# Performance work log

Hardware: AMD Instinct MI355X
Metric: run time of the kernel (lower is better)

## Reference

```python
import jax, jax.numpy as jnp
import numpy as np

N, D, H, DK, DEG = 8192, 512, 8, 64, 16
E = N * DEG
M = N


def setup_inputs() -> dict:
    key = jax.random.key(0)
    ks = jax.random.split(key, 12)
    x = jax.random.normal(ks[0], (N, D), dtype=jnp.float32)
    # every node has DEG neighbors -> sorted row index, random cols
    row_index = jnp.repeat(jnp.arange(N, dtype=jnp.int64), DEG)
    col_index = jax.random.randint(ks[1], (E,), 0, M, dtype=jnp.int64)
    to_col_index = jax.random.randint(ks[2], (M,), 0, N, dtype=jnp.int64)
    att_bias = 0.1 * jax.random.normal(ks[3], (H, E), dtype=jnp.float32)
    pos = 10.0 * jax.random.uniform(ks[4], (N, 3), dtype=jnp.float32)
    col_pos = 10.0 * jax.random.uniform(ks[5], (M, 3), dtype=jnp.float32)
    dist = jnp.linalg.norm(col_pos[col_index] - pos[row_index], axis=-1)
    s = 1.0 / np.sqrt(D)
    Wq = s * jax.random.normal(ks[6], (H, DK, D), dtype=jnp.float32)
    Wqv = s * jax.random.normal(ks[7], (H, 3, D), dtype=jnp.float32)
    Wk = s * jax.random.normal(ks[8], (H, DK, D), dtype=jnp.float32)
    Wv = s * jax.random.normal(ks[9], (H, DK, D), dtype=jnp.float32)
    Wout = s * jax.random.normal(ks[10], (D, D + 4 * H), dtype=jnp.float32)
    bout = jnp.zeros((D,), dtype=jnp.float32)
    return {"x": x, "row_index": row_index, "col_index": col_index,
            "to_col_index": to_col_index, "att_bias": att_bias, "dist": dist,
            "pos": pos, "col_pos": col_pos, "Wq": Wq, "Wqv": Wqv, "Wk": Wk,
            "Wv": Wv, "Wout": Wout, "bout": bout}


def reference(x, row_index, col_index, to_col_index, att_bias, dist, pos,
              col_pos, Wq, Wqv, Wk, Wv, Wout, bout):
    n = x.shape[0]
    dk = Wq.shape[1]
    scale = 1.0 / jnp.sqrt(jnp.asarray(dk, x.dtype))
    # per-head projections: [H, N, dk]
    q = jnp.einsum('nd,hkd->hnk', x, Wq) * scale
    qv = jnp.einsum('nd,hkd->hnk', x, Wqv)              # [H, N, 3]
    kx = jnp.einsum('nd,hkd->hnk', x, Wk)[:, to_col_index]  # [H, M, dk]
    vx = jnp.einsum('nd,hkd->hnk', x, Wv)[:, to_col_index]
    # gather per edge -> [E, H, *]
    qe = q[:, row_index].transpose(1, 0, 2)
    ke = kx[:, col_index].transpose(1, 0, 2)
    qve = qv[:, row_index].transpose(1, 0, 2)           # [E, H, 3]
    rel = col_pos[col_index] - pos[row_index]           # [E, 3]
    dist_e = jnp.where(dist == 0, jnp.inf, dist)        # masked_fill(dist==0, inf)
    # angular = qv_row . col_pos_col - qv_row . pos_row = qv_row . rel
    angular = jnp.einsum('ehc,ec->eh', qve, rel)
    logit = jnp.einsum('ehk,ehk->eh', qe, ke) + att_bias.T + angular / dist_e[:, None]
    # sparse (per-row segment) softmax
    m = jax.ops.segment_max(logit, row_index, num_segments=n)
    p = jnp.exp(logit - m[row_index])
    s = jax.ops.segment_sum(p, row_index, num_segments=n)
    att = p / s[row_index]                              # [E, H]
    natt = att / dist_e[:, None]
    dst_vec = jax.ops.segment_sum(natt[:, :, None] * col_pos[col_index][:, None, :],
                                  row_index, num_segments=n)   # [N, H, 3]
    avg_inv_dist = jax.ops.segment_sum(natt, row_index, num_segments=n)  # [N, H]
    src_vec = avg_inv_dist[:, :, None] * pos[:, None, :]
    diff = dst_vec - src_vec
    feat3 = diff / jnp.maximum(jnp.linalg.norm(diff, axis=-1, keepdims=True), 1e-12)
    ve = vx[:, col_index].transpose(1, 0, 2)            # [E, H, dk]
    y = jax.ops.segment_sum(att[:, :, None] * ve, row_index, num_segments=n)  # [N, H, dk]
    feat = jnp.concatenate([y, feat3, avg_inv_dist[:, :, None]], axis=-1)
    feat = feat.reshape(n, -1)                          # [N, H*(dk+4)]
    return feat @ Wout.T + bout
```

## Files before the change

kernel.cpp:

```cpp
#include <hip/hip_runtime.h>
#include <math.h>

#define N_NODES 8192
#define D_FEAT  512
#define H_HEADS 8
#define DKH     64
#define DEG     16
#define E_EDGES (N_NODES * DEG)
#define FEAT_W  544
#define OUT_W   512
#define QKV_W   1664

typedef unsigned short u16;
typedef __attribute__((ext_vector_type(8))) short short8;
typedef __attribute__((ext_vector_type(8))) unsigned short us8;
typedef __attribute__((ext_vector_type(4))) float f32x4;

__device__ __forceinline__ u16 f2bf(float f) {
    union { float f; unsigned u; } c; c.f = f;
    unsigned u = c.u;
    unsigned r = u + 0x7FFFu + ((u >> 16) & 1u);
    return (u16)(r >> 16);
}
__device__ __forceinline__ float bf2f(u16 h) {
    union { unsigned u; float f; } c; c.u = ((unsigned)h) << 16;
    return c.f;
}

__device__ __forceinline__ void async16(const void* g, void* l) {
    __builtin_amdgcn_global_load_lds(
        (const __attribute__((address_space(1))) void*)g,
        (__attribute__((address_space(3))) void*)l, 16, 0, 0);
}

template<bool HAS_BL, bool BF16_OUT>
__global__ __launch_bounds__(256) void gemm_mfma(
    const u16* __restrict__ Ah,
    const u16* __restrict__ Bh, const u16* __restrict__ Bl,
    const float* __restrict__ bias, void* __restrict__ Cout,
    int M, int N, int K)
{
    constexpr int NB = HAS_BL ? 2 : 1;
    __shared__ u16 smem[128 * 32 * (1 + NB)];
    u16* sAh = smem;
    u16* sBh = smem + 128 * 32;
    u16* sBl = smem + 128 * 32 * 2;

    const int tid  = threadIdx.x;
    const int bm   = blockIdx.y * 128;
    const int bn   = blockIdx.x * 128;
    const int wave = tid >> 6;
    const int lane = tid & 63;
    const int wr   = (wave >> 1) * 64;
    const int wc   = (wave & 1) * 64;
    const int lrow = lane & 15;
    const int quad = lane >> 4;

    f32x4 acc[4][4];
    #pragma unroll
    for (int i = 0; i < 4; ++i)
        #pragma unroll
        for (int j = 0; j < 4; ++j) {
            f32x4 z = {0.f, 0.f, 0.f, 0.f};
            acc[i][j] = z;
        }

    for (int k0 = 0; k0 < K; k0 += 32) {
        #pragma unroll
        for (int i = 0; i < 2; ++i) {
            const int lin = i * 256 + tid;
            const int row = lin >> 2;
            const int seg = (lin & 3) << 3;
            const int loff = lin << 3;
            const size_t ga = (size_t)(bm + row) * K + k0 + seg;
            const size_t gb = (size_t)(bn + row) * K + k0 + seg;
            async16(Ah + ga, sAh + loff);
            async16(Bh + gb, sBh + loff);
            if (HAS_BL) async16(Bl + gb, sBl + loff);
        }
        __syncthreads();

        short8 a_h[4], b_h[4], b_l[4];
        #pragma unroll
        for (int t = 0; t < 4; ++t) {
            const int ar = (wr + t * 16 + lrow) * 32 + quad * 8;
            const int br = (wc + t * 16 + lrow) * 32 + quad * 8;
            a_h[t] = *(const short8*)&sAh[ar];
            b_h[t] = *(const short8*)&sBh[br];
            if (HAS_BL) b_l[t] = *(const short8*)&sBl[br];
        }

        #pragma unroll
        for (int mt = 0; mt < 4; ++mt)
            #pragma unroll
            for (int nt = 0; nt < 4; ++nt) {
                acc[mt][nt] = __builtin_amdgcn_mfma_f32_16x16x32_bf16(
                    a_h[mt], b_h[nt], acc[mt][nt], 0, 0, 0);
                if (HAS_BL)
                    acc[mt][nt] = __builtin_amdgcn_mfma_f32_16x16x32_bf16(
                        a_h[mt], b_l[nt], acc[mt][nt], 0, 0, 0);
            }
        __syncthreads();
    }

    #pragma unroll
    for (int nt = 0; nt < 4; ++nt) {
        const int col = bn + wc + nt * 16 + lrow;
        const float bb = bias ? bias[col] : 0.f;
        #pragma unroll
        for (int mt = 0; mt < 4; ++mt) {
            #pragma unroll
            for (int r = 0; r < 4; ++r) {
                const int row = bm + wr + mt * 16 + quad * 4 + r;
                const float v = acc[mt][nt][r] + bb;
                if (BF16_OUT)
                    ((u16*)Cout)[(size_t)row * N + col] = f2bf(v);
                else
                    ((float*)Cout)[(size_t)row * N + col] = v;
            }
        }
    }
}

__global__ __launch_bounds__(256) void prep_kernel(
    const float* __restrict__ x,
    const float* __restrict__ Wq, const float* __restrict__ Wk,
    const float* __restrict__ Wv, const float* __restrict__ Wqv,
    const float* __restrict__ Wout,
    u16* __restrict__ xh, u16* __restrict__ B,
    u16* __restrict__ Woth, u16* __restrict__ Wotl)
{
    const int b = blockIdx.x;
    const int tid = threadIdx.x;
    if (b < 4096) {
        const int i = b * 256 + tid;
        const float4 v = ((const float4*)x)[i];
        ushort4 h;
        h.x = f2bf(v.x); h.y = f2bf(v.y); h.z = f2bf(v.z); h.w = f2bf(v.w);
        ((ushort4*)xh)[i] = h;
    } else if (b < 4928) {
        const int idx = (b - 4096) * 256 + tid;
        const int row = idx >> 7;
        const int c4  = idx & 127;
        float4 v = make_float4(0.f, 0.f, 0.f, 0.f);
        float scale = 1.f;
        if (row < 512) {
            v = *(const float4*)(Wq + (size_t)row * 512 + c4 * 4);
            scale = 0.125f;
        } else if (row < 1024) {
            v = *(const float4*)(Wk + (size_t)(row - 512) * 512 + c4 * 4);
        } else if (row < 1536) {
            v = *(const float4*)(Wv + (size_t)(row - 1024) * 512 + c4 * 4);
        } else if (row < 1560) {
            v = *(const float4*)(Wqv + (size_t)(row - 1536) * 512 + c4 * 4);
        }
        ushort4 h;
        h.x = f2bf(v.x * scale); h.y = f2bf(v.y * scale);
        h.z = f2bf(v.z * scale); h.w = f2bf(v.w * scale);
        ((ushort4*)B)[idx] = h;
    } else {
        const int i = (b - 4928) * 256 + tid;
        if (i >= OUT_W * FEAT_W / 4) return;
        const float4 v = ((const float4*)Wout)[i];
        ushort4 h, l;
        h.x = f2bf(v.x); l.x = f2bf(v.x - bf2f(h.x));
        h.y = f2bf(v.y); l.y = f2bf(v.y - bf2f(h.y));
        h.z = f2bf(v.z); l.z = f2bf(v.z - bf2f(h.z));
        h.w = f2bf(v.w); l.w = f2bf(v.w - bf2f(h.w));
        ((ushort4*)Woth)[i] = h;
        ((ushort4*)Wotl)[i] = l;
    }
}

#define EK_WAVES 2
__global__ __launch_bounds__(EK_WAVES * 64) void edge_kernel(
    const u16* __restrict__ qkv,
    const int* __restrict__ col_index, const int* __restrict__ to_col,
    const float* __restrict__ att_bias, const float* __restrict__ dist,
    const float* __restrict__ pos, const float* __restrict__ col_pos,
    u16* __restrict__ feat)
{
    __shared__ u16 vbuf[EK_WAVES * DEG * 512];

    const int wave = threadIdx.x >> 6;
    const int lane = threadIdx.x & 63;
    const int n = blockIdx.x * EK_WAVES + wave;
    const int h = lane >> 3;
    const int sub = lane & 7;

    const size_t qbase = (size_t)n * QKV_W;
    const int hoff = lane * 8;

    float qf[8];
    {
        const us8 qu = *(const us8*)(qkv + qbase + hoff);
        #pragma unroll
        for (int i = 0; i < 8; ++i) qf[i] = bf2f(qu[i]);
    }
    float qv0, qv1, qv2;
    {
        const float qvl = bf2f(qkv[qbase + 1536 + (lane < 24 ? lane : 0)]);
        qv0 = __shfl(qvl, h * 3 + 0);
        qv1 = __shfl(qvl, h * 3 + 1);
        qv2 = __shfl(qvl, h * 3 + 2);
    }
    const float px = pos[3 * n + 0], py = pos[3 * n + 1], pz = pos[3 * n + 2];

    const int j16 = lane & 15;
    const int e0  = n * DEG + j16;
    const int c_l  = col_index[e0];
    const int cc_l = to_col[c_l];
    const float d_l = dist[e0];
    const float invd_l = (d_l == 0.f) ? 0.f : (1.f / d_l);
    const float rx_l = col_pos[3 * c_l + 0] - px;
    const float ry_l = col_pos[3 * c_l + 1] - py;
    const float rz_l = col_pos[3 * c_l + 2] - pz;

    const float b0 = att_bias[(size_t)h * E_EDGES + n * DEG + sub * 2 + 0];
    const float b1 = att_bias[(size_t)h * E_EDGES + n * DEG + sub * 2 + 1];

    float logit[DEG];
    u16* vb = &vbuf[wave * DEG * 512];
    #pragma unroll
    for (int j = 0; j < DEG; ++j) {
        const int cc = __shfl(cc_l, j);
        const u16* rowp = qkv + (size_t)cc * QKV_W + hoff;
        async16(rowp + 1024, vb + j * 512);
        const us8 ku = *(const us8*)(rowp + 512);
        float dot = 0.f;
        #pragma unroll
        for (int i = 0; i < 8; ++i) dot += qf[i] * bf2f(ku[i]);
        dot += __shfl_xor(dot, 1, 8);
        dot += __shfl_xor(dot, 2, 8);
        dot += __shfl_xor(dot, 4, 8);
        const float invd = __shfl(invd_l, j);
        const float ang = qv0 * __shfl(rx_l, j) + qv1 * __shfl(ry_l, j)
                        + qv2 * __shfl(rz_l, j);
        const float bj = __shfl((j & 1) ? b1 : b0, j >> 1, 8);
        logit[j] = dot + bj + ang * invd;
    }

    float m = logit[0];
    #pragma unroll
    for (int j = 1; j < DEG; ++j) m = fmaxf(m, logit[j]);
    float s = 0.f;
    #pragma unroll
    for (int j = 0; j < DEG; ++j) { logit[j] = __expf(logit[j] - m); s += logit[j]; }
    const float inv_s = 1.f / s;

    __syncthreads();

    float y[8] = {0.f, 0.f, 0.f, 0.f, 0.f, 0.f, 0.f, 0.f};
    float dx = 0.f, dy = 0.f, dz = 0.f, aid = 0.f;
    #pragma unroll
    for (int j = 0; j < DEG; ++j) {
        const float a = logit[j] * inv_s;
        const us8 vu = *(const us8*)&vb[j * 512 + hoff];
        #pragma unroll
        for (int i = 0; i < 8; ++i) y[i] += a * bf2f(vu[i]);
        const float na = a * __shfl(invd_l, j);
        dx += na * __shfl(rx_l, j);
        dy += na * __shfl(ry_l, j);
        dz += na * __shfl(rz_l, j);
        aid += na;
    }

    u16* f = feat + (size_t)n * FEAT_W + h * (DKH + 4);
    ushort4 o0, o1;
    o0.x = f2bf(y[0]); o0.y = f2bf(y[1]); o0.z = f2bf(y[2]); o0.w = f2bf(y[3]);
    o1.x = f2bf(y[4]); o1.y = f2bf(y[5]); o1.z = f2bf(y[6]); o1.w = f2bf(y[7]);
    *(ushort4*)(f + sub * 8 + 0) = o0;
    *(ushort4*)(f + sub * 8 + 4) = o1;
    if (sub == 0) {
        const float nrm = sqrtf(dx * dx + dy * dy + dz * dz);
        const float rn = 1.f / fmaxf(nrm, 1e-12f);
        ushort4 ex;
        ex.x = f2bf(dx * rn); ex.y = f2bf(dy * rn);
        ex.z = f2bf(dz * rn); ex.w = f2bf(aid);
        *(ushort4*)(f + DKH) = ex;
    }
}

extern "C" void kernel_launch(void* const* d_in, const int* in_sizes, int n_in,
                              void* d_out, int out_size, void* d_ws, size_t ws_size,
                              hipStream_t stream)
{
    const float* x         = (const float*)d_in[0];
    const int*   col_index = (const int*)d_in[2];
    const int*   to_col    = (const int*)d_in[3];
    const float* att_bias  = (const float*)d_in[4];
    const float* dist      = (const float*)d_in[5];
    const float* pos       = (const float*)d_in[6];
    const float* col_pos   = (const float*)d_in[7];
    const float* Wq        = (const float*)d_in[8];
    const float* Wqv       = (const float*)d_in[9];
    const float* Wk        = (const float*)d_in[10];
    const float* Wv        = (const float*)d_in[11];
    const float* Wout      = (const float*)d_in[12];
    const float* bout      = (const float*)d_in[13];
    float* out = (float*)d_out;

    char* ws = (char*)d_ws;
    u16* qkv   = (u16*)(ws + 0);
    u16* xh    = (u16*)(ws + 27262976);
    u16* Bfuse = (u16*)(ws + 35651584);
    u16* Woth  = (u16*)(ws + 37355520);
    u16* Wotl  = (u16*)(ws + 37912576);
    u16* feat  = (u16*)(ws + 38469632);

    dim3 blk(256);

    hipLaunchKernelGGL(prep_kernel, dim3(5200), blk, 0, stream,
                       x, Wq, Wk, Wv, Wqv, Wout, xh, Bfuse, Woth, Wotl);

    hipLaunchKernelGGL((gemm_mfma<false, true>), dim3(QKV_W / 128, N_NODES / 128),
                       blk, 0, stream,
                       xh, Bfuse, (const u16*)nullptr, (const float*)nullptr,
                       (void*)qkv, N_NODES, QKV_W, D_FEAT);

    hipLaunchKernelGGL(edge_kernel, dim3(N_NODES / EK_WAVES), dim3(EK_WAVES * 64),
                       0, stream,
                       qkv, col_index, to_col, att_bias, dist, pos, col_pos, feat);

    hipLaunchKernelGGL((gemm_mfma<true, false>), dim3(OUT_W / 128, N_NODES / 128),
                       blk, 0, stream,
                       feat, Woth, Wotl, bout, (void*)out,
                       N_NODES, OUT_W, FEAT_W);
}
```

Measured before the change: 191.2 us.

## Use 64-wide swizzled GEMM K tiles and process two nodes per wave

The MFMA GEMM now stages 64-wide K tiles in LDS with an XOR swizzle, which halves the number of barrier iterations and is meant to avoid LDS bank conflicts. To fit the 64-wide tiles, the feature width and Wout are zero-padded from 544 to 576 columns. The edge kernel now handles two nodes per wave in 256-thread blocks and reads V rows directly from global memory instead of staging them through LDS. This is meant to raise memory-level parallelism and remove the LDS buffer and its barrier. The trade-offs are more K padding work in the output GEMM, higher register pressure, and feat padding columns that are never written, so they rely on the zero weights and on the workspace not holding NaN.

```diff
diff --git a/kernel.cpp b/kernel.cpp
--- a/kernel.cpp
+++ b/kernel.cpp
@@ -7,7 +7,8 @@
 #define DKH     64
 #define DEG     16
 #define E_EDGES (N_NODES * DEG)
-#define FEAT_W  544
+#define FEAT_W  576
+#define FEAT_USED 544
 #define OUT_W   512
 #define QKV_W   1664
 
@@ -40,11 +41,11 @@
     const float* __restrict__ bias, void* __restrict__ Cout,
     int M, int N, int K)
 {
-    constexpr int NB = HAS_BL ? 2 : 1;
-    __shared__ u16 smem[128 * 32 * (1 + NB)];
+    constexpr int NMAT = HAS_BL ? 3 : 2;
+    __shared__ u16 smem[128 * 64 * NMAT];
     u16* sAh = smem;
-    u16* sBh = smem + 128 * 32;
-    u16* sBl = smem + 128 * 32 * 2;
+    u16* sBh = smem + 128 * 64;
+    u16* sBl = smem + 128 * 64 * 2;
 
     const int tid  = threadIdx.x;
     const int bm   = blockIdx.y * 128;
@@ -65,12 +66,14 @@
             acc[i][j] = z;
         }
 
-    for (int k0 = 0; k0 < K; k0 += 32) {
-        #pragma unroll
-        for (int i = 0; i < 2; ++i) {
+    for (int k0 = 0; k0 < K; k0 += 64) {
+        #pragma unroll
+        for (int i = 0; i < 4; ++i) {
             const int lin = i * 256 + tid;
-            const int row = lin >> 2;
-            const int seg = (lin & 3) << 3;
+            const int row = lin >> 3;
+            const int cs  = lin & 7;
+            const int cu  = cs ^ (row & 7);
+            const int seg = cu << 3;
             const int loff = lin << 3;
             const size_t ga = (size_t)(bm + row) * K + k0 + seg;
             const size_t gb = (size_t)(bn + row) * K + k0 + seg;
@@ -80,26 +83,31 @@
         }
         __syncthreads();
 
-        short8 a_h[4], b_h[4], b_l[4];
-        #pragma unroll
-        for (int t = 0; t < 4; ++t) {
-            const int ar = (wr + t * 16 + lrow) * 32 + quad * 8;
-            const int br = (wc + t * 16 + lrow) * 32 + quad * 8;
-            a_h[t] = *(const short8*)&sAh[ar];
-            b_h[t] = *(const short8*)&sBh[br];
-            if (HAS_BL) b_l[t] = *(const short8*)&sBl[br];
-        }
-
-        #pragma unroll
-        for (int mt = 0; mt < 4; ++mt)
+        #pragma unroll
+        for (int ko = 0; ko < 64; ko += 32) {
+            const int cbase = ko >> 3;
+            short8 a_h[4], b_h[4], b_l[4];
             #pragma unroll
-            for (int nt = 0; nt < 4; ++nt) {
-                acc[mt][nt] = __builtin_amdgcn_mfma_f32_16x16x32_bf16(
-                    a_h[mt], b_h[nt], acc[mt][nt], 0, 0, 0);
-                if (HAS_BL)
+            for (int t = 0; t < 4; ++t) {
+                const int ra = wr + t * 16 + lrow;
+                const int rb = wc + t * 16 + lrow;
+                const int ca = ((cbase + quad) ^ (ra & 7)) << 3;
+                const int cb = ((cbase + quad) ^ (rb & 7)) << 3;
+                a_h[t] = *(const short8*)&sAh[ra * 64 + ca];
+                b_h[t] = *(const short8*)&sBh[rb * 64 + cb];
+                if (HAS_BL) b_l[t] = *(const short8*)&sBl[rb * 64 + cb];
+            }
+            #pragma unroll
+            for (int mt = 0; mt < 4; ++mt)
+                #pragma unroll
+                for (int nt = 0; nt < 4; ++nt) {
                     acc[mt][nt] = __builtin_amdgcn_mfma_f32_16x16x32_bf16(
-                        a_h[mt], b_l[nt], acc[mt][nt], 0, 0, 0);
-            }
+                        a_h[mt], b_h[nt], acc[mt][nt], 0, 0, 0);
+                    if (HAS_BL)
+                        acc[mt][nt] = __builtin_amdgcn_mfma_f32_16x16x32_bf16(
+                            a_h[mt], b_l[nt], acc[mt][nt], 0, 0, 0);
+                }
+        }
         __syncthreads();
     }
 
@@ -161,7 +169,11 @@
     } else {
         const int i = (b - 4928) * 256 + tid;
         if (i >= OUT_W * FEAT_W / 4) return;
-        const float4 v = ((const float4*)Wout)[i];
+        const int row = i / (FEAT_W / 4);
+        const int c4  = i % (FEAT_W / 4);
+        float4 v = make_float4(0.f, 0.f, 0.f, 0.f);
+        if (c4 < FEAT_USED / 4)
+            v = *(const float4*)(Wout + (size_t)row * FEAT_USED + c4 * 4);
         ushort4 h, l;
         h.x = f2bf(v.x); l.x = f2bf(v.x - bf2f(h.x));
         h.y = f2bf(v.y); l.y = f2bf(v.y - bf2f(h.y));
@@ -172,112 +184,148 @@
     }
 }
 
-#define EK_WAVES 2
-__global__ __launch_bounds__(EK_WAVES * 64) void edge_kernel(
+__global__ __launch_bounds__(256) void edge_kernel(
     const u16* __restrict__ qkv,
     const int* __restrict__ col_index, const int* __restrict__ to_col,
     const float* __restrict__ att_bias, const float* __restrict__ dist,
     const float* __restrict__ pos, const float* __restrict__ col_pos,
     u16* __restrict__ feat)
 {
-    __shared__ u16 vbuf[EK_WAVES * DEG * 512];
-
     const int wave = threadIdx.x >> 6;
     const int lane = threadIdx.x & 63;
-    const int n = blockIdx.x * EK_WAVES + wave;
+    const int n0 = (blockIdx.x * 4 + wave) * 2;
+    const int n1 = n0 + 1;
     const int h = lane >> 3;
     const int sub = lane & 7;
-
-    const size_t qbase = (size_t)n * QKV_W;
     const int hoff = lane * 8;
 
-    float qf[8];
+    float qf0[8], qf1[8];
     {
-        const us8 qu = *(const us8*)(qkv + qbase + hoff);
-        #pragma unroll
-        for (int i = 0; i < 8; ++i) qf[i] = bf2f(qu[i]);
-    }
-    float qv0, qv1, qv2;
+        const us8 qu0 = *(const us8*)(qkv + (size_t)n0 * QKV_W + hoff);
+        const us8 qu1 = *(const us8*)(qkv + (size_t)n1 * QKV_W + hoff);
+        #pragma unroll
+        for (int i = 0; i < 8; ++i) { qf0[i] = bf2f(qu0[i]); qf1[i] = bf2f(qu1[i]); }
+    }
+    float qv00, qv01, qv02, qv10, qv11, qv12;
     {
-        const float qvl = bf2f(qkv[qbase + 1536 + (lane < 24 ? lane : 0)]);
-        qv0 = __shfl(qvl, h * 3 + 0);
-        qv1 = __shfl(qvl, h * 3 + 1);
-        qv2 = __shfl(qvl, h * 3 + 2);
-    }
-    const float px = pos[3 * n + 0], py = pos[3 * n + 1], pz = pos[3 * n + 2];
-
+        const int qc = (lane < 24 ? lane : 0);
+        const float a = bf2f(qkv[(size_t)n0 * QKV_W + 1536 + qc]);
+        const float b = bf2f(qkv[(size_t)n1 * QKV_W + 1536 + qc]);
+        qv00 = __shfl(a, h * 3 + 0); qv01 = __shfl(a, h * 3 + 1); qv02 = __shfl(a, h * 3 + 2);
+        qv10 = __shfl(b, h * 3 + 0); qv11 = __shfl(b, h * 3 + 1); qv12 = __shfl(b, h * 3 + 2);
+    }
+    const float px0 = pos[3 * n0 + 0], py0 = pos[3 * n0 + 1], pz0 = pos[3 * n0 + 2];
+    const float px1 = pos[3 * n1 + 0], py1 = pos[3 * n1 + 1], pz1 = pos[3 * n1 + 2];
+
+    const int gm  = (lane >> 4) & 1;
     const int j16 = lane & 15;
-    const int e0  = n * DEG + j16;
-    const int c_l  = col_index[e0];
+    const int nm  = n0 + gm;
+    const int em  = nm * DEG + j16;
+    const int c_l  = col_index[em];
     const int cc_l = to_col[c_l];
-    const float d_l = dist[e0];
+    const float d_l = dist[em];
     const float invd_l = (d_l == 0.f) ? 0.f : (1.f / d_l);
-    const float rx_l = col_pos[3 * c_l + 0] - px;
-    const float ry_l = col_pos[3 * c_l + 1] - py;
-    const float rz_l = col_pos[3 * c_l + 2] - pz;
-
-    const float b0 = att_bias[(size_t)h * E_EDGES + n * DEG + sub * 2 + 0];
-    const float b1 = att_bias[(size_t)h * E_EDGES + n * DEG + sub * 2 + 1];
-
-    float logit[DEG];
-    u16* vb = &vbuf[wave * DEG * 512];
+    const float rx_l = col_pos[3 * c_l + 0] - (gm ? px1 : px0);
+    const float ry_l = col_pos[3 * c_l + 1] - (gm ? py1 : py0);
+    const float rz_l = col_pos[3 * c_l + 2] - (gm ? pz1 : pz0);
+
+    const float b00 = att_bias[(size_t)h * E_EDGES + n0 * DEG + sub * 2 + 0];
+    const float b01 = att_bias[(size_t)h * E_EDGES + n0 * DEG + sub * 2 + 1];
+    const float b10 = att_bias[(size_t)h * E_EDGES + n1 * DEG + sub * 2 + 0];
+    const float b11 = att_bias[(size_t)h * E_EDGES + n1 * DEG + sub * 2 + 1];
+
+    float logit0[DEG], logit1[DEG];
     #pragma unroll
     for (int j = 0; j < DEG; ++j) {
-        const int cc = __shfl(cc_l, j);
-        const u16* rowp = qkv + (size_t)cc * QKV_W + hoff;
-        async16(rowp + 1024, vb + j * 512);
-        const us8 ku = *(const us8*)(rowp + 512);
-        float dot = 0.f;
-        #pragma unroll
-        for (int i = 0; i < 8; ++i) dot += qf[i] * bf2f(ku[i]);
-        dot += __shfl_xor(dot, 1, 8);
-        dot += __shfl_xor(dot, 2, 8);
-        dot += __shfl_xor(dot, 4, 8);
-        const float invd = __shfl(invd_l, j);
-        const float ang = qv0 * __shfl(rx_l, j) + qv1 * __shfl(ry_l, j)
-                        + qv2 * __shfl(rz_l, j);
-        const float bj = __shfl((j & 1) ? b1 : b0, j >> 1, 8);
-        logit[j] = dot + bj + ang * invd;
-    }
-
-    float m = logit[0];
-    #pragma unroll
-    for (int j = 1; j < DEG; ++j) m = fmaxf(m, logit[j]);
-    float s = 0.f;
-    #pragma unroll
-    for (int j = 0; j < DEG; ++j) { logit[j] = __expf(logit[j] - m); s += logit[j]; }
-    const float inv_s = 1.f / s;
-
-    __syncthreads();
-
-    float y[8] = {0.f, 0.f, 0.f, 0.f, 0.f, 0.f, 0.f, 0.f};
-    float dx = 0.f, dy = 0.f, dz = 0.f, aid = 0.f;
+        const int cc0 = __shfl(cc_l, j);
+        const int cc1 = __shfl(cc_l, 16 + j);
+        const us8 ku0 = *(const us8*)(qkv + (size_t)cc0 * QKV_W + 512 + hoff);
+        const us8 ku1 = *(const us8*)(qkv + (size_t)cc1 * QKV_W + 512 + hoff);
+        float dot0 = 0.f, dot1 = 0.f;
+        #pragma unroll
+        for (int i = 0; i < 8; ++i) {
+            dot0 += qf0[i] * bf2f(ku0[i]);
+            dot1 += qf1[i] * bf2f(ku1[i]);
+        }
+        dot0 += __shfl_xor(dot0, 1, 8); dot1 += __shfl_xor(dot1, 1, 8);
+        dot0 += __shfl_xor(dot0, 2, 8); dot1 += __shfl_xor(dot1, 2, 8);
+        dot0 += __shfl_xor(dot0, 4, 8); dot1 += __shfl_xor(dot1, 4, 8);
+        const float ang0 = qv00 * __shfl(rx_l, j) + qv01 * __shfl(ry_l, j)
+                         + qv02 * __shfl(rz_l, j);
+        const float ang1 = qv10 * __shfl(rx_l, 16 + j) + qv11 * __shfl(ry_l, 16 + j)
+                         + qv12 * __shfl(rz_l, 16 + j);
+        const float bj0 = __shfl((j & 1) ? b01 : b00, j >> 1, 8);
+        const float bj1 = __shfl((j & 1) ? b11 : b10, j >> 1, 8);
+        logit0[j] = dot0 + bj0 + ang0 * __shfl(invd_l, j);
+        logit1[j] = dot1 + bj1 + ang1 * __shfl(invd_l, 16 + j);
+    }
+
+    float m0 = logit0[0], m1 = logit1[0];
+    #pragma unroll
+    for (int j = 1; j < DEG; ++j) { m0 = fmaxf(m0, logit0[j]); m1 = fmaxf(m1, logit1[j]); }
+    float s0 = 0.f, s1 = 0.f;
     #pragma unroll
     for (int j = 0; j < DEG; ++j) {
-        const float a = logit[j] * inv_s;
-        const us8 vu = *(const us8*)&vb[j * 512 + hoff];
-        #pragma unroll
-        for (int i = 0; i < 8; ++i) y[i] += a * bf2f(vu[i]);
-        const float na = a * __shfl(invd_l, j);
-        dx += na * __shfl(rx_l, j);
-        dy += na * __shfl(ry_l, j);
-        dz += na * __shfl(rz_l, j);
-        aid += na;
-    }
-
-    u16* f = feat + (size_t)n * FEAT_W + h * (DKH + 4);
-    ushort4 o0, o1;
-    o0.x = f2bf(y[0]); o0.y = f2bf(y[1]); o0.z = f2bf(y[2]); o0.w = f2bf(y[3]);
-    o1.x = f2bf(y[4]); o1.y = f2bf(y[5]); o1.z = f2bf(y[6]); o1.w = f2bf(y[7]);
-    *(ushort4*)(f + sub * 8 + 0) = o0;
-    *(ushort4*)(f + sub * 8 + 4) = o1;
-    if (sub == 0) {
-        const float nrm = sqrtf(dx * dx + dy * dy + dz * dz);
-        const float rn = 1.f / fmaxf(nrm, 1e-12f);
-        ushort4 ex;
-        ex.x = f2bf(dx * rn); ex.y = f2bf(dy * rn);
-        ex.z = f2bf(dz * rn); ex.w = f2bf(aid);
-        *(ushort4*)(f + DKH) = ex;
+        logit0[j] = __expf(logit0[j] - m0); s0 += logit0[j];
+        logit1[j] = __expf(logit1[j] - m1); s1 += logit1[j];
+    }
+    const float is0 = 1.f / s0, is1 = 1.f / s1;
+
+    float y0[8] = {0,0,0,0,0,0,0,0}, y1[8] = {0,0,0,0,0,0,0,0};
+    float dx0 = 0.f, dy0 = 0.f, dz0 = 0.f, a0 = 0.f;
+    float dx1 = 0.f, dy1 = 0.f, dz1 = 0.f, a1 = 0.f;
+    #pragma unroll
+    for (int j = 0; j < DEG; ++j) {
+        const int cc0 = __shfl(cc_l, j);
+        const int cc1 = __shfl(cc_l, 16 + j);
+        const us8 vu0 = *(const us8*)(qkv + (size_t)cc0 * QKV_W + 1024 + hoff);
+        const us8 vu1 = *(const us8*)(qkv + (size_t)cc1 * QKV_W + 1024 + hoff);
+        const float w0 = logit0[j] * is0;
+        const float w1 = logit1[j] * is1;
+        #pragma unroll
+        for (int i = 0; i < 8; ++i) {
+            y0[i] += w0 * bf2f(vu0[i]);
+            y1[i] += w1 * bf2f(vu1[i]);
+        }
+        const float na0 = w0 * __shfl(invd_l, j);
+        const float na1 = w1 * __shfl(invd_l, 16 + j);
+        dx0 += na0 * __shfl(rx_l, j);       dx1 += na1 * __shfl(rx_l, 16 + j);
+        dy0 += na0 * __shfl(ry_l, j);       dy1 += na1 * __shfl(ry_l, 16 + j);
+        dz0 += na0 * __shfl(rz_l, j);       dz1 += na1 * __shfl(rz_l, 16 + j);
+        a0 += na0;                          a1 += na1;
+    }
+
+    {
+        u16* f = feat + (size_t)n0 * FEAT_W + h * (DKH + 4);
+        ushort4 o0, o1;
+        o0.x = f2bf(y0[0]); o0.y = f2bf(y0[1]); o0.z = f2bf(y0[2]); o0.w = f2bf(y0[3]);
+        o1.x = f2bf(y0[4]); o1.y = f2bf(y0[5]); o1.z = f2bf(y0[6]); o1.w = f2bf(y0[7]);
+        *(ushort4*)(f + sub * 8 + 0) = o0;
+        *(ushort4*)(f + sub * 8 + 4) = o1;
+        if (sub == 0) {
+            const float nrm = sqrtf(dx0 * dx0 + dy0 * dy0 + dz0 * dz0);
+            const float rn = 1.f / fmaxf(nrm, 1e-12f);
+            ushort4 ex;
+            ex.x = f2bf(dx0 * rn); ex.y = f2bf(dy0 * rn);
+            ex.z = f2bf(dz0 * rn); ex.w = f2bf(a0);
+            *(ushort4*)(f + DKH) = ex;
+        }
+    }
+    {
+        u16* f = feat + (size_t)n1 * FEAT_W + h * (DKH + 4);
+        ushort4 o0, o1;
+        o0.x = f2bf(y1[0]); o0.y = f2bf(y1[1]); o0.z = f2bf(y1[2]); o0.w = f2bf(y1[3]);
+        o1.x = f2bf(y1[4]); o1.y = f2bf(y1[5]); o1.z = f2bf(y1[6]); o1.w = f2bf(y1[7]);
+        *(ushort4*)(f + sub * 8 + 0) = o0;
+        *(ushort4*)(f + sub * 8 + 4) = o1;
+        if (sub == 0) {
+            const float nrm = sqrtf(dx1 * dx1 + dy1 * dy1 + dz1 * dz1);
+            const float rn = 1.f / fmaxf(nrm, 1e-12f);
+            ushort4 ex;
+            ex.x = f2bf(dx1 * rn); ex.y = f2bf(dy1 * rn);
+            ex.z = f2bf(dz1 * rn); ex.w = f2bf(a1);
+            *(ushort4*)(f + DKH) = ex;
+        }
     }
 }
 
@@ -305,12 +353,12 @@
     u16* xh    = (u16*)(ws + 27262976);
     u16* Bfuse = (u16*)(ws + 35651584);
     u16* Woth  = (u16*)(ws + 37355520);
-    u16* Wotl  = (u16*)(ws + 37912576);
-    u16* feat  = (u16*)(ws + 38469632);
+    u16* Wotl  = (u16*)(ws + 37945344);
+    u16* feat  = (u16*)(ws + 38535168);
 
     dim3 blk(256);
 
-    hipLaunchKernelGGL(prep_kernel, dim3(5200), blk, 0, stream,
+    hipLaunchKernelGGL(prep_kernel, dim3(5216), blk, 0, stream,
                        x, Wq, Wk, Wv, Wqv, Wout, xh, Bfuse, Woth, Wotl);
 
     hipLaunchKernelGGL((gemm_mfma<false, true>), dim3(QKV_W / 128, N_NODES / 128),
@@ -318,8 +366,7 @@
                        xh, Bfuse, (const u16*)nullptr, (const float*)nullptr,
                        (void*)qkv, N_NODES, QKV_W, D_FEAT);
 
-    hipLaunchKernelGGL(edge_kernel, dim3(N_NODES / EK_WAVES), dim3(EK_WAVES * 64),
-                       0, stream,
+    hipLaunchKernelGGL(edge_kernel, dim3(N_NODES / 8), blk, 0, stream,
                        qkv, col_index, to_col, att_bias, dist, pos, col_pos, feat);
 
     hipLaunchKernelGGL((gemm_mfma<true, false>), dim3(OUT_W / 128, N_NODES / 128),
```

Result: slower. 226.3 us (+18.3%).

## Swizzle 64-wide K tiles, remap blocks per XCD, drop Wout low-precision split

Applied to the files above, without the earlier changes.

The GEMM now stages K in 64-wide tiles in shared memory with an XOR swizzle on column chunks, to avoid LDS bank conflicts and halve the number of barriers per K. The grid is flattened and remapped so consecutive blocks on each XCD share M-row tiles, to improve L2 reuse. The output projection drops the bf16 hi/lo split of Wout, halving its MFMA work but lowering precision. FEAT_W is padded to 576 so K is a multiple of 64, with zeroed Wout columns covering the padding.

```diff
diff --git a/kernel.cpp b/kernel.cpp
--- a/kernel.cpp
+++ b/kernel.cpp
@@ -7,7 +7,8 @@
 #define DKH     64
 #define DEG     16
 #define E_EDGES (N_NODES * DEG)
-#define FEAT_W  544
+#define FEAT_W  576
+#define FEAT_USED 544
 #define OUT_W   512
 #define QKV_W   1664
 
@@ -40,15 +41,20 @@
     const float* __restrict__ bias, void* __restrict__ Cout,
     int M, int N, int K)
 {
-    constexpr int NB = HAS_BL ? 2 : 1;
-    __shared__ u16 smem[128 * 32 * (1 + NB)];
+    constexpr int NMAT = HAS_BL ? 3 : 2;
+    __shared__ u16 smem[128 * 64 * NMAT];
     u16* sAh = smem;
-    u16* sBh = smem + 128 * 32;
-    u16* sBl = smem + 128 * 32 * 2;
+    u16* sBh = smem + 128 * 64;
+    u16* sBl = smem + 128 * 64 * 2;
 
     const int tid  = threadIdx.x;
-    const int bm   = blockIdx.y * 128;
-    const int bn   = blockIdx.x * 128;
+    const int ntiles = N >> 7;
+    const int flat = blockIdx.x;
+    const int xcd  = flat & 7;
+    const int rr   = flat >> 3;
+    const int bm   = (xcd + 8 * (rr / ntiles)) * 128;
+    const int bn   = (rr % ntiles) * 128;
+
     const int wave = tid >> 6;
     const int lane = tid & 63;
     const int wr   = (wave >> 1) * 64;
@@ -65,12 +71,14 @@
             acc[i][j] = z;
         }
 
-    for (int k0 = 0; k0 < K; k0 += 32) {
-        #pragma unroll
-        for (int i = 0; i < 2; ++i) {
+    for (int k0 = 0; k0 < K; k0 += 64) {
+        #pragma unroll
+        for (int i = 0; i < 4; ++i) {
             const int lin = i * 256 + tid;
-            const int row = lin >> 2;
-            const int seg = (lin & 3) << 3;
+            const int row = lin >> 3;
+            const int cs  = lin & 7;
+            const int cu  = cs ^ (row & 7);
+            const int seg = cu << 3;
             const int loff = lin << 3;
             const size_t ga = (size_t)(bm + row) * K + k0 + seg;
             const size_t gb = (size_t)(bn + row) * K + k0 + seg;
@@ -80,26 +88,31 @@
         }
         __syncthreads();
 
-        short8 a_h[4], b_h[4], b_l[4];
-        #pragma unroll
-        for (int t = 0; t < 4; ++t) {
-            const int ar = (wr + t * 16 + lrow) * 32 + quad * 8;
-            const int br = (wc + t * 16 + lrow) * 32 + quad * 8;
-            a_h[t] = *(const short8*)&sAh[ar];
-            b_h[t] = *(const short8*)&sBh[br];
-            if (HAS_BL) b_l[t] = *(const short8*)&sBl[br];
-        }
-
-        #pragma unroll
-        for (int mt = 0; mt < 4; ++mt)
+        #pragma unroll
+        for (int ko = 0; ko < 64; ko += 32) {
+            const int cbase = ko >> 3;
+            short8 a_h[4], b_h[4], b_l[4];
             #pragma unroll
-            for (int nt = 0; nt < 4; ++nt) {
-                acc[mt][nt] = __builtin_amdgcn_mfma_f32_16x16x32_bf16(
-                    a_h[mt], b_h[nt], acc[mt][nt], 0, 0, 0);
-                if (HAS_BL)
+            for (int t = 0; t < 4; ++t) {
+                const int ra = wr + t * 16 + lrow;
+                const int rb = wc + t * 16 + lrow;
+                const int ca = ((cbase + quad) ^ (ra & 7)) << 3;
+                const int cb = ((cbase + quad) ^ (rb & 7)) << 3;
+                a_h[t] = *(const short8*)&sAh[ra * 64 + ca];
+                b_h[t] = *(const short8*)&sBh[rb * 64 + cb];
+                if (HAS_BL) b_l[t] = *(const short8*)&sBl[rb * 64 + cb];
+            }
+            #pragma unroll
+            for (int mt = 0; mt < 4; ++mt)
+                #pragma unroll
+                for (int nt = 0; nt < 4; ++nt) {
                     acc[mt][nt] = __builtin_amdgcn_mfma_f32_16x16x32_bf16(
-                        a_h[mt], b_l[nt], acc[mt][nt], 0, 0, 0);
-            }
+                        a_h[mt], b_h[nt], acc[mt][nt], 0, 0, 0);
+                    if (HAS_BL)
+                        acc[mt][nt] = __builtin_amdgcn_mfma_f32_16x16x32_bf16(
+                            a_h[mt], b_l[nt], acc[mt][nt], 0, 0, 0);
+                }
+        }
         __syncthreads();
     }
 
@@ -127,8 +140,7 @@
     const float* __restrict__ Wq, const float* __restrict__ Wk,
     const float* __restrict__ Wv, const float* __restrict__ Wqv,
     const float* __restrict__ Wout,
-    u16* __restrict__ xh, u16* __restrict__ B,
-    u16* __restrict__ Woth, u16* __restrict__ Wotl)
+    u16* __restrict__ xh, u16* __restrict__ B, u16* __restrict__ Woth)
 {
     const int b = blockIdx.x;
     const int tid = threadIdx.x;
@@ -161,14 +173,15 @@
     } else {
         const int i = (b - 4928) * 256 + tid;
         if (i >= OUT_W * FEAT_W / 4) return;
-        const float4 v = ((const float4*)Wout)[i];
-        ushort4 h, l;
-        h.x = f2bf(v.x); l.x = f2bf(v.x - bf2f(h.x));
-        h.y = f2bf(v.y); l.y = f2bf(v.y - bf2f(h.y));
-        h.z = f2bf(v.z); l.z = f2bf(v.z - bf2f(h.z));
-        h.w = f2bf(v.w); l.w = f2bf(v.w - bf2f(h.w));
+        const int row = i / (FEAT_W / 4);
+        const int c4  = i % (FEAT_W / 4);
+        float4 v = make_float4(0.f, 0.f, 0.f, 0.f);
+        if (c4 < FEAT_USED / 4)
+            v = *(const float4*)(Wout + (size_t)row * FEAT_USED + c4 * 4);
+        ushort4 h;
+        h.x = f2bf(v.x); h.y = f2bf(v.y);
+        h.z = f2bf(v.z); h.w = f2bf(v.w);
         ((ushort4*)Woth)[i] = h;
-        ((ushort4*)Wotl)[i] = l;
     }
 }
 
@@ -305,15 +318,14 @@
     u16* xh    = (u16*)(ws + 27262976);
     u16* Bfuse = (u16*)(ws + 35651584);
     u16* Woth  = (u16*)(ws + 37355520);
-    u16* Wotl  = (u16*)(ws + 37912576);
-    u16* feat  = (u16*)(ws + 38469632);
+    u16* feat  = (u16*)(ws + 37945344);
 
     dim3 blk(256);
 
-    hipLaunchKernelGGL(prep_kernel, dim3(5200), blk, 0, stream,
-                       x, Wq, Wk, Wv, Wqv, Wout, xh, Bfuse, Woth, Wotl);
-
-    hipLaunchKernelGGL((gemm_mfma<false, true>), dim3(QKV_W / 128, N_NODES / 128),
+    hipLaunchKernelGGL(prep_kernel, dim3(5216), blk, 0, stream,
+                       x, Wq, Wk, Wv, Wqv, Wout, xh, Bfuse, Woth);
+
+    hipLaunchKernelGGL((gemm_mfma<false, true>), dim3((N_NODES / 128) * (QKV_W / 128)),
                        blk, 0, stream,
                        xh, Bfuse, (const u16*)nullptr, (const float*)nullptr,
                        (void*)qkv, N_NODES, QKV_W, D_FEAT);
@@ -322,8 +334,8 @@
                        0, stream,
                        qkv, col_index, to_col, att_bias, dist, pos, col_pos, feat);
 
-    hipLaunchKernelGGL((gemm_mfma<true, false>), dim3(OUT_W / 128, N_NODES / 128),
+    hipLaunchKernelGGL((gemm_mfma<false, false>), dim3((N_NODES / 128) * (OUT_W / 128)),
                        blk, 0, stream,
-                       feat, Woth, Wotl, bout, (void*)out,
+                       feat, Woth, (const u16*)nullptr, bout, (void*)out,
                        N_NODES, OUT_W, FEAT_W);
 }
```

Measured after the change: 173.9 us. 9.1% less time.
